# Performance work log

Hardware: AMD Instinct MI355X
Metric: run time of the kernel (lower is better)

The kernel has to match this reference:

```python
import jax, jax.numpy as jnp
import numpy as np

B, S, I, H, O, L = 256, 512, 256, 256, 256, 64


def setup_inputs() -> dict:
    key = jax.random.key(0)
    ks = jax.random.split(key, 12)
    def lin(k, fan_in, fan_out):
        kw, kb = jax.random.split(k)
        lim = 1.0 / np.sqrt(fan_in)
        W = jax.random.uniform(kw, (fan_in, fan_out), jnp.float32, -lim, lim)
        b = jax.random.uniform(kb, (fan_out,), jnp.float32, -lim, lim)
        return W, b
    x = jax.random.normal(ks[0], (B, S, I), jnp.float32)
    W1x, b1x = lin(ks[1], I, H)   # rnn1.Wax
    W1a, b1a = lin(ks[2], H, H)   # rnn1.Waa
    W2x, b2x = lin(ks[3], O, H)   # rnn2.Wax
    W2a, b2a = lin(ks[4], H, H)   # rnn2.Waa
    Wy, by = lin(ks[5], H, O)     # Wya
    return {"x": x, "W1x": W1x, "b1x": b1x, "W1a": W1a, "b1a": b1a,
            "W2x": W2x, "b2x": b2x, "W2a": W2a, "b2a": b2a, "Wy": Wy, "by": by}


def reference(x, W1x, b1x, W1a, b1a, W2x, b2x, W2a, b2a, Wy, by):
    batch = x.shape[0]
    a0 = jnp.zeros((batch, W1a.shape[0]), x.dtype)  # a[:, -1] is zeros at encoder start

    # Encoder: a_t = tanh(Wax(x_t) + Waa(a_{t-1}))
    def enc_step(a, x_t):
        a = jnp.tanh(x_t @ W1x + b1x + a @ W1a + b1a)
        return a, None
    a_last, _ = jax.lax.scan(enc_step, a0, jnp.swapaxes(x, 0, 1))  # [S,B,I] scan

    # Torch code: y_pred[:,0] set from encoder, then decoder reads y_pred[:,i]
    # BEFORE overwriting it -> input is y0 at i=0, zeros for i>0.
    y0 = jax.nn.sigmoid(a_last @ Wy + by)  # [B,O]
    zero_in = jnp.zeros_like(y0)

    def dec_step(a, i):
        inp = jnp.where(i == 0, y0, zero_in)
        a = jnp.tanh(inp @ W2x + b2x + a @ W2a + b2a)
        y = jax.nn.sigmoid(a @ Wy + by)
        return a, y
    _, ys = jax.lax.scan(dec_step, a_last, jnp.arange(L))  # ys: [L,B,O]
    return jnp.swapaxes(ys, 0, 1)  # [B,L,O]
```

## Files before the change

kernel.cpp:

```cpp
#include <hip/hip_runtime.h>

typedef unsigned short u16;
typedef unsigned int   u32;
typedef __attribute__((ext_vector_type(8))) __bf16 bf16x8;
typedef __attribute__((ext_vector_type(8))) u16    u16x8;
typedef __attribute__((ext_vector_type(4))) float  f32x4;
typedef __attribute__((ext_vector_type(4))) u32    u32x4;
typedef __attribute__((ext_vector_type(2))) u32    u32x2;

#define MFMA16(a,b,c) __builtin_amdgcn_mfma_f32_16x16x32_bf16((a),(b),(c),0,0,0)
#define C_TANH 2.8853900817779268f
#define NL2E  -1.4426950408889634f

__device__ __forceinline__ float ubit(u32 x){ return __builtin_bit_cast(float, x); }
__device__ __forceinline__ u16 f2b(float f){
    u32 b = __builtin_bit_cast(u32, f);
    b += 0x7FFFu + ((b >> 16) & 1u);
    return (u16)(b >> 16);
}
__device__ __forceinline__ u32 pkbf(float a, float b){ return ((u32)f2b(b) << 16) | (u32)f2b(a); }
__device__ __forceinline__ u32 pk_away(float a, float b){
    u32 ua = (__builtin_bit_cast(u32, a) + 0x8000u) >> 16;
    u32 ub = (__builtin_bit_cast(u32, b) + 0x8000u) & 0xFFFF0000u;
    return ub | ua;
}
__device__ __forceinline__ void bar_lds(){ __asm__ volatile("s_waitcnt lgkmcnt(0)\n\ts_barrier" ::: "memory"); }

__global__ __launch_bounds__(256, 1) void k1_xw(const float* __restrict__ x, const float* __restrict__ w1x,
                                               const float* __restrict__ b1x, const float* __restrict__ b1a,
                                               u16* __restrict__ xpre)
{
    const int t = blockIdx.x;
    const int tid = threadIdx.x, lane = tid & 63, w = tid >> 6;
    const int l15 = lane & 15, q = lane >> 4;
    const int cw = w * 64;

    bf16x8 bw[4][8];
    f32x4 biasv[4];
    #pragma unroll
    for (int nt = 0; nt < 4; ++nt){
        const int n0 = cw + nt * 16 + q * 4;
        f32x4 bx = *(const f32x4*)(b1x + n0);
        f32x4 ba = *(const f32x4*)(b1a + n0);
        biasv[nt] = (bx + ba) * C_TANH;
        const int n = cw + nt * 16 + l15;
        #pragma unroll
        for (int ks = 0; ks < 8; ++ks){
            u16x8 tt;
            #pragma unroll
            for (int j = 0; j < 8; ++j) tt[j] = f2b(w1x[(ks * 32 + q * 8 + j) * 256 + n] * C_TANH);
            bw[nt][ks] = __builtin_bit_cast(bf16x8, tt);
        }
    }

    for (int blk = 0; blk < 16; ++blk){
        const int b0r = blk * 16;
        bf16x8 av[8];
        #pragma unroll
        for (int ks = 0; ks < 8; ++ks){
            const float* p = x + ((size_t)(b0r + l15) * 512 + t) * 256 + ks * 32 + q * 8;
            f32x4 v0 = *(const f32x4*)p;
            f32x4 v1 = *(const f32x4*)(p + 4);
            u32x4 dd = { pkbf(v0[0], v0[1]), pkbf(v0[2], v0[3]),
                         pkbf(v1[0], v1[1]), pkbf(v1[2], v1[3]) };
            av[ks] = __builtin_bit_cast(bf16x8, dd);
        }
        f32x4 acc[4];
        #pragma unroll
        for (int nt = 0; nt < 4; ++nt) acc[nt] = biasv[nt];
        #pragma unroll
        for (int ks = 0; ks < 8; ++ks)
            #pragma unroll
            for (int nt = 0; nt < 4; ++nt)
                acc[nt] = MFMA16(bw[nt][ks], av[ks], acc[nt]);
        const int bg = blk * 4 + (l15 >> 2), b4 = l15 & 3;
        #pragma unroll
        for (int p2 = 0; p2 < 2; ++p2){
            const size_t a16 = ((((size_t)t * 64 + bg) * 8 + (w * 2 + p2)) * 16 + q * 4 + b4) * 8;
            u32x4 V = { pkbf(acc[p2 * 2][0], acc[p2 * 2][1]), pkbf(acc[p2 * 2][2], acc[p2 * 2][3]),
                        pkbf(acc[p2 * 2 + 1][0], acc[p2 * 2 + 1][1]), pkbf(acc[p2 * 2 + 1][2], acc[p2 * 2 + 1][3]) };
            *(u32x4*)(xpre + a16) = V;
        }
    }
}

__global__ __launch_bounds__(512, 2) void k2_full(const float* __restrict__ w1a, const float* __restrict__ wy,
                                                 const float* __restrict__ by,  const float* __restrict__ w2x,
                                                 const float* __restrict__ w2a, const float* __restrict__ b2x,
                                                 const float* __restrict__ b2a, u16* ws)
{
    __shared__ __align__(16) u16 st[2][4][272];
    const int tid = threadIdx.x, lane = tid & 63, w = tid >> 6;
    const int l15 = lane & 15, q = lane >> 4;
    const int b4 = l15 & 3;
    const bool selnt = (l15 & 4) != 0, selrp = (l15 & 8) != 0;
    const int wcol = w * 32 + (selnt ? 16 : 0) + q * 4 + (selrp ? 2 : 0);
    const int bg = blockIdx.x;

    bf16x8 bw[2][8];
    #pragma unroll
    for (int nt = 0; nt < 2; ++nt){
        const int n = w * 32 + nt * 16 + l15;
        #pragma unroll
        for (int ks = 0; ks < 8; ++ks){
            u16x8 tt;
            #pragma unroll
            for (int j = 0; j < 8; ++j) tt[j] = f2b(w1a[(ks * 32 + q * 8 + j) * 256 + n] * C_TANH);
            bw[nt][ks] = __builtin_bit_cast(bf16x8, tt);
        }
    }
    for (int i = tid; i < 4 * 272; i += 512) (&st[0][0][0])[i] = 0;
    __syncthreads();

    const u16* xp = ws + (((size_t)bg * 8 + w) * 16 + q * 4 + b4) * 8;
    u32x4 c = *(const u32x4*)xp;
    u32x4 a = *(const u32x4*)(xp + 65536);

    const u16 (*sR)[272] = st[0];
    u16 (*sW)[272] = st[1];

    for (int t = 0; t < 512; ++t){
        const size_t tp = (size_t)((t + 2 < 512) ? t + 2 : 511) * 65536;
        u32x4 n_ = *(const u32x4*)(xp + tp);

        bf16x8 av[8];
        #pragma unroll
        for (int ks = 0; ks < 8; ++ks)
            av[ks] = *(const bf16x8*)&sR[b4][ks * 32 + q * 8];

        f32x4 acc[2];
        #pragma unroll
        for (int nt = 0; nt < 2; ++nt)
            #pragma unroll
            for (int r = 0; r < 4; ++r){
                const u32 d = c[nt * 2 + (r >> 1)];
                acc[nt][r] = ubit((r & 1) ? (d & 0xFFFF0000u) : (d << 16));
            }
        __builtin_amdgcn_s_setprio(1);
        #pragma unroll
        for (int ks = 0; ks < 8; ++ks)
            #pragma unroll
            for (int nt = 0; nt < 2; ++nt)
                acc[nt] = MFMA16(bw[nt][ks], av[ks], acc[nt]);
        __builtin_amdgcn_s_setprio(0);

        const float s0 = selnt ? acc[1][0] : acc[0][0];
        const float s1 = selnt ? acc[1][1] : acc[0][1];
        const float s2 = selnt ? acc[1][2] : acc[0][2];
        const float s3 = selnt ? acc[1][3] : acc[0][3];
        const float mv0 = selrp ? s2 : s0;
        const float mv1 = selrp ? s3 : s1;
        const float e0 = __builtin_amdgcn_exp2f(mv0);
        const float t0 = 1.0f - 2.0f * __builtin_amdgcn_rcpf(e0 + 1.0f);
        const float e1 = __builtin_amdgcn_exp2f(mv1);
        const float t1 = 1.0f - 2.0f * __builtin_amdgcn_rcpf(e1 + 1.0f);
        *(u32*)&sW[b4][wcol] = pk_away(t0, t1);

        c = a; a = n_;
        bar_lds();
        const u16 (*tmp)[272] = sR; sR = (const u16(*)[272])sW; sW = (u16(*)[272])tmp;
    }

    {
        bf16x8 bwy[2][8];
        f32x4 biasy[2];
        #pragma unroll
        for (int nt = 0; nt < 2; ++nt){
            const int n0 = w * 32 + nt * 16 + q * 4;
            biasy[nt] = (*(const f32x4*)(by + n0)) * NL2E;
            const int n = w * 32 + nt * 16 + l15;
            #pragma unroll
            for (int ks = 0; ks < 8; ++ks){
                u16x8 tt;
                #pragma unroll
                for (int j = 0; j < 8; ++j) tt[j] = f2b(wy[(ks * 32 + q * 8 + j) * 256 + n] * NL2E);
                bwy[nt][ks] = __builtin_bit_cast(bf16x8, tt);
            }
        }
        bf16x8 av[8];
        #pragma unroll
        for (int ks = 0; ks < 8; ++ks) av[ks] = *(const bf16x8*)&sR[b4][ks * 32 + q * 8];
        f32x4 acc[2];
        #pragma unroll
        for (int nt = 0; nt < 2; ++nt) acc[nt] = biasy[nt];
        #pragma unroll
        for (int ks = 0; ks < 8; ++ks)
            #pragma unroll
            for (int nt = 0; nt < 2; ++nt) acc[nt] = MFMA16(bwy[nt][ks], av[ks], acc[nt]);
        const float s0 = selnt ? acc[1][0] : acc[0][0];
        const float s1 = selnt ? acc[1][1] : acc[0][1];
        const float s2 = selnt ? acc[1][2] : acc[0][2];
        const float s3 = selnt ? acc[1][3] : acc[0][3];
        const float mv0 = selrp ? s2 : s0;
        const float mv1 = selrp ? s3 : s1;
        const float y0v = __builtin_amdgcn_rcpf(1.0f + __builtin_amdgcn_exp2f(mv0));
        const float y1v = __builtin_amdgcn_rcpf(1.0f + __builtin_amdgcn_exp2f(mv1));
        *(u32*)&sW[b4][wcol] = pkbf(y0v, y1v);
    }
    bar_lds();

    f32x4 ini[2];
    f32x4 bias2[2];
    {
        bf16x8 av2[8];
        #pragma unroll
        for (int ks = 0; ks < 8; ++ks) av2[ks] = *(const bf16x8*)&sW[b4][ks * 32 + q * 8];
        bar_lds();
        #pragma unroll
        for (int nt = 0; nt < 2; ++nt){
            const int n0 = w * 32 + nt * 16 + q * 4;
            f32x4 bx = *(const f32x4*)(b2x + n0);
            f32x4 ba = *(const f32x4*)(b2a + n0);
            bias2[nt] = (bx + ba) * C_TANH;
            ini[nt] = (f32x4){0.f, 0.f, 0.f, 0.f};
        }
        #pragma unroll
        for (int ks = 0; ks < 8; ++ks)
            #pragma unroll
            for (int nt = 0; nt < 2; ++nt){
                const int n = w * 32 + nt * 16 + l15;
                u16x8 tt;
                #pragma unroll
                for (int j = 0; j < 8; ++j) tt[j] = f2b(w2x[(ks * 32 + q * 8 + j) * 256 + n] * C_TANH);
                ini[nt] = MFMA16(__builtin_bit_cast(bf16x8, tt), av2[ks], ini[nt]);
            }
        #pragma unroll
        for (int nt = 0; nt < 2; ++nt) ini[nt] = ini[nt] + bias2[nt];
        #pragma unroll
        for (int nt = 0; nt < 2; ++nt){
            const int n = w * 32 + nt * 16 + l15;
            #pragma unroll
            for (int ks = 0; ks < 8; ++ks){
                u16x8 tt;
                #pragma unroll
                for (int j = 0; j < 8; ++j) tt[j] = f2b(w2a[(ks * 32 + q * 8 + j) * 256 + n] * C_TANH);
                bw[nt][ks] = __builtin_bit_cast(bf16x8, tt);
            }
        }
    }

    for (int i = 0; i < 64; ++i){
        bf16x8 av[8];
        #pragma unroll
        for (int ks = 0; ks < 8; ++ks) av[ks] = *(const bf16x8*)&sR[b4][ks * 32 + q * 8];
        f32x4 acc[2];
        #pragma unroll
        for (int nt = 0; nt < 2; ++nt) acc[nt] = ini[nt];
        __builtin_amdgcn_s_setprio(1);
        #pragma unroll
        for (int ks = 0; ks < 8; ++ks)
            #pragma unroll
            for (int nt = 0; nt < 2; ++nt) acc[nt] = MFMA16(bw[nt][ks], av[ks], acc[nt]);
        __builtin_amdgcn_s_setprio(0);

        const float s0 = selnt ? acc[1][0] : acc[0][0];
        const float s1 = selnt ? acc[1][1] : acc[0][1];
        const float s2 = selnt ? acc[1][2] : acc[0][2];
        const float s3 = selnt ? acc[1][3] : acc[0][3];
        const float mv0 = selrp ? s2 : s0;
        const float mv1 = selrp ? s3 : s1;
        const float e0 = __builtin_amdgcn_exp2f(mv0);
        const float t0 = 1.0f - 2.0f * __builtin_amdgcn_rcpf(e0 + 1.0f);
        const float e1 = __builtin_amdgcn_exp2f(mv1);
        const float t1 = 1.0f - 2.0f * __builtin_amdgcn_rcpf(e1 + 1.0f);
        const u32 hp = pk_away(t0, t1);
        *(u32*)&sW[b4][wcol] = hp;
        *(u32*)(ws + (((size_t)(i * 64 + bg)) << 10) + b4 * 256 + wcol) = hp;

        if (i == 0){
            #pragma unroll
            for (int nt = 0; nt < 2; ++nt) ini[nt] = bias2[nt];
        }
        bar_lds();
        const u16 (*tmp)[272] = sR; sR = (const u16(*)[272])sW; sW = (u16(*)[272])tmp;
    }
}

__global__ __launch_bounds__(256, 1) void k3_out(const float* __restrict__ wy, const float* __restrict__ by,
                                                const u16* __restrict__ astate, float* __restrict__ out)
{
    const int tid = threadIdx.x, lane = tid & 63, w = tid >> 6;
    const int l15 = lane & 15, q = lane >> 4;

    bf16x8 bwy[4][8];
    f32x4 biasy[4];
    #pragma unroll
    for (int nt = 0; nt < 4; ++nt){
        const int n0 = w * 64 + nt * 16 + q * 4;
        biasy[nt] = (*(const f32x4*)(by + n0)) * NL2E;
        const int n = w * 64 + nt * 16 + l15;
        #pragma unroll
        for (int ks = 0; ks < 8; ++ks){
            u16x8 tt;
            #pragma unroll
            for (int j = 0; j < 8; ++j) tt[j] = f2b(wy[(ks * 32 + q * 8 + j) * 256 + n] * NL2E);
            bwy[nt][ks] = __builtin_bit_cast(bf16x8, tt);
        }
    }
    #pragma unroll
    for (int tix = 0; tix < 4; ++tix){
        const int R0 = (blockIdx.x * 4 + tix) * 16;
        const int Rl = R0 + l15, iiL = Rl >> 8, bL = Rl & 255;
        const u16* ap = astate + (((size_t)(iiL * 64 + (bL >> 2))) << 10) + (size_t)(bL & 3) * 256;
        bf16x8 av[8];
        #pragma unroll
        for (int ks = 0; ks < 8; ++ks)
            av[ks] = *(const bf16x8*)(ap + ks * 32 + q * 8);
        f32x4 acc[4];
        #pragma unroll
        for (int nt = 0; nt < 4; ++nt) acc[nt] = biasy[nt];
        #pragma unroll
        for (int ks = 0; ks < 8; ++ks)
            #pragma unroll
            for (int nt = 0; nt < 4; ++nt) acc[nt] = MFMA16(bwy[nt][ks], av[ks], acc[nt]);
        #pragma unroll
        for (int nt = 0; nt < 4; ++nt){
            f32x4 o4;
            #pragma unroll
            for (int r = 0; r < 4; ++r)
                o4[r] = __builtin_amdgcn_rcpf(1.0f + __builtin_amdgcn_exp2f(acc[nt][r]));
            *(f32x4*)(out + ((size_t)bL * 64 + iiL) * 256 + w * 64 + nt * 16 + q * 4) = o4;
        }
    }
}

extern "C" void kernel_launch(void* const* d_in, const int* in_sizes, int n_in,
                              void* d_out, int out_size, void* d_ws, size_t ws_size,
                              hipStream_t stream) {
    const float* x   = (const float*)d_in[0];
    const float* w1x = (const float*)d_in[1];
    const float* b1x = (const float*)d_in[2];
    const float* w1a = (const float*)d_in[3];
    const float* b1a = (const float*)d_in[4];
    const float* w2x = (const float*)d_in[5];
    const float* b2x = (const float*)d_in[6];
    const float* w2a = (const float*)d_in[7];
    const float* b2a = (const float*)d_in[8];
    const float* wy  = (const float*)d_in[9];
    const float* by  = (const float*)d_in[10];

    u16*   ws16 = (u16*)d_ws;
    float* o    = (float*)d_out;

    k1_xw  <<<512, 256, 0, stream>>>(x, w1x, b1x, b1a, ws16);
    k2_full<<<64,  512, 0, stream>>>(w1a, wy, by, w2x, w2a, b2x, b2a, ws16);
    k3_out <<<256, 256, 0, stream>>>(wy, by, ws16, o);
}
```

Measured before the change: 534.0 us.

## Fuse output projection into recurrent kernel and pack two timesteps per k1 block

The separate output kernel k3 is removed. Each recurrent block now computes the Wy projection and sigmoid for its own batch group after the decoder loop, reading back the hidden states it wrote to the workspace. The Wy weights are hoisted out of the encoder-tail scope so they are loaded only once. k1 now launches 256 blocks of 512 threads, each block handling two timesteps. This saves a kernel launch and avoids re-converting the weights, but the 64 k2 blocks must now do all 64x256 output rows themselves, with less parallelism than the 256-block k3 had.

```diff
diff --git a/kernel.cpp b/kernel.cpp
--- a/kernel.cpp
+++ b/kernel.cpp
@@ -26,12 +26,14 @@
 }
 __device__ __forceinline__ void bar_lds(){ __asm__ volatile("s_waitcnt lgkmcnt(0)\n\ts_barrier" ::: "memory"); }
 
-__global__ __launch_bounds__(256, 1) void k1_xw(const float* __restrict__ x, const float* __restrict__ w1x,
+__global__ __launch_bounds__(512, 2) void k1_xw(const float* __restrict__ x, const float* __restrict__ w1x,
                                                const float* __restrict__ b1x, const float* __restrict__ b1a,
                                                u16* __restrict__ xpre)
 {
-    const int t = blockIdx.x;
-    const int tid = threadIdx.x, lane = tid & 63, w = tid >> 6;
+    const int tid = threadIdx.x, lane = tid & 63;
+    const int w8 = tid >> 6;
+    const int wg2 = w8 >> 2, w = w8 & 3;
+    const int t = blockIdx.x * 2 + wg2;
     const int l15 = lane & 15, q = lane >> 4;
     const int cw = w * 64;
 
@@ -87,7 +89,8 @@
 __global__ __launch_bounds__(512, 2) void k2_full(const float* __restrict__ w1a, const float* __restrict__ wy,
                                                  const float* __restrict__ by,  const float* __restrict__ w2x,
                                                  const float* __restrict__ w2a, const float* __restrict__ b2x,
-                                                 const float* __restrict__ b2a, u16* ws)
+                                                 const float* __restrict__ b2a, u16* ws,
+                                                 float* __restrict__ out)
 {
     __shared__ __align__(16) u16 st[2][4][272];
     const int tid = threadIdx.x, lane = tid & 63, w = tid >> 6;
@@ -161,22 +164,22 @@
         const u16 (*tmp)[272] = sR; sR = (const u16(*)[272])sW; sW = (u16(*)[272])tmp;
     }
 
+    bf16x8 bwy[2][8];
+    f32x4 biasy[2];
+    #pragma unroll
+    for (int nt = 0; nt < 2; ++nt){
+        const int n0 = w * 32 + nt * 16 + q * 4;
+        biasy[nt] = (*(const f32x4*)(by + n0)) * NL2E;
+        const int n = w * 32 + nt * 16 + l15;
+        #pragma unroll
+        for (int ks = 0; ks < 8; ++ks){
+            u16x8 tt;
+            #pragma unroll
+            for (int j = 0; j < 8; ++j) tt[j] = f2b(wy[(ks * 32 + q * 8 + j) * 256 + n] * NL2E);
+            bwy[nt][ks] = __builtin_bit_cast(bf16x8, tt);
+        }
+    }
     {
-        bf16x8 bwy[2][8];
-        f32x4 biasy[2];
-        #pragma unroll
-        for (int nt = 0; nt < 2; ++nt){
-            const int n0 = w * 32 + nt * 16 + q * 4;
-            biasy[nt] = (*(const f32x4*)(by + n0)) * NL2E;
-            const int n = w * 32 + nt * 16 + l15;
-            #pragma unroll
-            for (int ks = 0; ks < 8; ++ks){
-                u16x8 tt;
-                #pragma unroll
-                for (int j = 0; j < 8; ++j) tt[j] = f2b(wy[(ks * 32 + q * 8 + j) * 256 + n] * NL2E);
-                bwy[nt][ks] = __builtin_bit_cast(bf16x8, tt);
-            }
-        }
         bf16x8 av[8];
         #pragma unroll
         for (int ks = 0; ks < 8; ++ks) av[ks] = *(const bf16x8*)&sR[b4][ks * 32 + q * 8];
@@ -274,52 +277,35 @@
         bar_lds();
         const u16 (*tmp)[272] = sR; sR = (const u16(*)[272])sW; sW = (u16(*)[272])tmp;
     }
-}
-
-__global__ __launch_bounds__(256, 1) void k3_out(const float* __restrict__ wy, const float* __restrict__ by,
-                                                const u16* __restrict__ astate, float* __restrict__ out)
-{
-    const int tid = threadIdx.x, lane = tid & 63, w = tid >> 6;
-    const int l15 = lane & 15, q = lane >> 4;
-
-    bf16x8 bwy[4][8];
-    f32x4 biasy[4];
-    #pragma unroll
-    for (int nt = 0; nt < 4; ++nt){
-        const int n0 = w * 64 + nt * 16 + q * 4;
-        biasy[nt] = (*(const f32x4*)(by + n0)) * NL2E;
-        const int n = w * 64 + nt * 16 + l15;
-        #pragma unroll
-        for (int ks = 0; ks < 8; ++ks){
-            u16x8 tt;
-            #pragma unroll
-            for (int j = 0; j < 8; ++j) tt[j] = f2b(wy[(ks * 32 + q * 8 + j) * 256 + n] * NL2E);
-            bwy[nt][ks] = __builtin_bit_cast(bf16x8, tt);
-        }
-    }
-    #pragma unroll
-    for (int tix = 0; tix < 4; ++tix){
-        const int R0 = (blockIdx.x * 4 + tix) * 16;
-        const int Rl = R0 + l15, iiL = Rl >> 8, bL = Rl & 255;
-        const u16* ap = astate + (((size_t)(iiL * 64 + (bL >> 2))) << 10) + (size_t)(bL & 3) * 256;
+
+    __asm__ volatile("s_waitcnt vmcnt(0)" ::: "memory");
+    __syncthreads();
+    const int ib4 = l15 & 3;
+    const int ri4 = l15 >> 2;
+    for (int rt = 0; rt < 16; ++rt){
+        const int ii = rt * 4 + ri4;
+        const u16* ap = ws + (((size_t)(ii * 64 + bg)) << 10) + (size_t)ib4 * 256;
         bf16x8 av[8];
         #pragma unroll
         for (int ks = 0; ks < 8; ++ks)
             av[ks] = *(const bf16x8*)(ap + ks * 32 + q * 8);
-        f32x4 acc[4];
-        #pragma unroll
-        for (int nt = 0; nt < 4; ++nt) acc[nt] = biasy[nt];
-        #pragma unroll
-        for (int ks = 0; ks < 8; ++ks)
-            #pragma unroll
-            for (int nt = 0; nt < 4; ++nt) acc[nt] = MFMA16(bwy[nt][ks], av[ks], acc[nt]);
-        #pragma unroll
-        for (int nt = 0; nt < 4; ++nt){
+        f32x4 acc[2];
+        #pragma unroll
+        for (int nt = 0; nt < 2; ++nt) acc[nt] = biasy[nt];
+        __builtin_amdgcn_s_setprio(1);
+        #pragma unroll
+        for (int ks = 0; ks < 8; ++ks)
+            #pragma unroll
+            for (int nt = 0; nt < 2; ++nt) acc[nt] = MFMA16(bwy[nt][ks], av[ks], acc[nt]);
+        __builtin_amdgcn_s_setprio(0);
+        const int bL = bg * 4 + ib4;
+        #pragma unroll
+        for (int nt = 0; nt < 2; ++nt){
             f32x4 o4;
             #pragma unroll
             for (int r = 0; r < 4; ++r)
                 o4[r] = __builtin_amdgcn_rcpf(1.0f + __builtin_amdgcn_exp2f(acc[nt][r]));
-            *(f32x4*)(out + ((size_t)bL * 64 + iiL) * 256 + w * 64 + nt * 16 + q * 4) = o4;
+            *(f32x4*)(out + ((size_t)bL * 64 + ii) * 256 + w * 32 + nt * 16 + q * 4) = o4;
         }
     }
 }
@@ -342,7 +328,6 @@
     u16*   ws16 = (u16*)d_ws;
     float* o    = (float*)d_out;
 
-    k1_xw  <<<512, 256, 0, stream>>>(x, w1x, b1x, b1a, ws16);
-    k2_full<<<64,  512, 0, stream>>>(w1a, wy, by, w2x, w2a, b2x, b2a, ws16);
-    k3_out <<<256, 256, 0, stream>>>(wy, by, ws16, o);
-}
+    k1_xw  <<<256, 512, 0, stream>>>(x, w1x, b1x, b1a, ws16);
+    k2_full<<<64,  512, 0, stream>>>(w1a, wy, by, w2x, w2a, b2x, b2a, ws16, o);
+}
```

Result: slower. 603.9 us (+13.1%).
